# Kernel tuning notes

Hardware: AMD Instinct MI355X
Metric: run time of the kernel (lower is better)

The kernel has to match this reference:

```python
import jax, jax.numpy as jnp
import numpy as np

N = 1_000_000
D_IN = 128
D_OUT = 64
NUM_CLASSES = 64


def setup_inputs() -> dict:
    key = jax.random.key(0)
    k1, k2, k3, k4 = jax.random.split(key, 4)
    inputs = jax.random.normal(k1, (N, D_IN), dtype=jnp.float32)
    labels = jax.random.randint(k2, (N,), 0, NUM_CLASSES, dtype=jnp.int32)
    # Linear embedding parameters
    W = jax.random.normal(k3, (D_IN, D_OUT), dtype=jnp.float32) / np.sqrt(D_IN)
    b = jax.random.normal(k4, (D_OUT,), dtype=jnp.float32) * 0.01
    return {"inputs": inputs, "labels": labels, "W": W, "b": b}


def reference(inputs, labels, W, b):
    # embedding: simple linear map  [N, D_IN] -> [N, D_OUT]
    emb = jnp.einsum("nd,de->ne", inputs, W) + b
    # per-class mean pooling (prototype): segment sum / segment count
    seg_sum = jax.ops.segment_sum(emb, labels, num_segments=NUM_CLASSES)  # [C, D_OUT]
    counts = jax.ops.segment_sum(jnp.ones((inputs.shape[0],), dtype=emb.dtype),
                                 labels, num_segments=NUM_CLASSES)  # [C]
    protos = seg_sum / jnp.maximum(counts, 1.0)[:, None]
    return protos
```

## Files before the change

### kernel.cpp

```cpp
#include <hip/hip_runtime.h>

#define C_CLASSES 64
#define D_IN 128
#define D_OUT 64
#define CHUNK 32
#define CHUNK_FLTS (CHUNK * D_IN)
#define GSUM_FLTS (C_CLASSES * D_IN)
#define NBLK 1024


typedef __attribute__((ext_vector_type(8))) __bf16 bf16x8;
typedef __attribute__((ext_vector_type(8))) unsigned short us8;
typedef __attribute__((ext_vector_type(4))) float f32x4;

union frag_cast { us8 u; bf16x8 b; };

__device__ __forceinline__ unsigned short f2bf(float f) {
    unsigned u = __float_as_uint(f);
    unsigned r = u + 0x7FFFu + ((u >> 16) & 1u);
    return (unsigned short)(r >> 16);
}

__device__ __forceinline__ void stage16(const float* g, float* l) {
    __builtin_amdgcn_global_load_lds(
        (const __attribute__((address_space(1))) unsigned int*)g,
        (__attribute__((address_space(3))) unsigned int*)l, 16, 0, 0);
}

__global__ __launch_bounds__(256) void seg_mm_kernel(
    const float* __restrict__ x, const int* __restrict__ labels,
    float* __restrict__ gsum, float* __restrict__ partials, int n)
{
    __shared__ float buf[2][CHUNK_FLTS];

    const int lane = threadIdx.x & 63;
    const int wave = threadIdx.x >> 6;
    const int n16  = lane & 15;
    const int quad = lane >> 4;
    const int cb   = wave * 32;

    f32x4 acc[4][2];
#pragma unroll
    for (int t = 0; t < 4; ++t)
#pragma unroll
        for (int u = 0; u < 2; ++u)
            acc[t][u] = (f32x4){0.f, 0.f, 0.f, 0.f};

    const int stride = (int)gridDim.x * CHUNK;
    const int rb0    = (int)blockIdx.x * CHUNK;
    const int lslice = wave * 256;
    const int gslice = lslice + lane * 4;

#pragma unroll
    for (int r = 0; r < 4; ++r)
        stage16(x + (size_t)rb0 * D_IN + r * 1024 + gslice,
                &buf[0][r * 1024 + lslice]);
    int4 pl0 = *(const int4*)(labels + rb0 + quad * 8);
    int4 pl1 = *(const int4*)(labels + rb0 + quad * 8 + 4);

    int bufi = 0;
    for (int rb = rb0; rb < n; rb += stride, bufi ^= 1) {
        const int rbn = rb + stride;
        const bool hasNext = rbn < n;
        int4 pn0, pn1;
        if (hasNext) {
#pragma unroll
            for (int r = 0; r < 4; ++r)
                stage16(x + (size_t)rbn * D_IN + r * 1024 + gslice,
                        &buf[bufi ^ 1][r * 1024 + lslice]);
            pn0 = *(const int4*)(labels + rbn + quad * 8);
            pn1 = *(const int4*)(labels + rbn + quad * 8 + 4);
        }

        if (hasNext) {
            asm volatile("s_waitcnt vmcnt(6)\n\ts_barrier" ::: "memory");
        } else {
            asm volatile("s_waitcnt vmcnt(0)\n\ts_barrier" ::: "memory");
        }

        const int labv[8] = {pl0.x, pl0.y, pl0.z, pl0.w,
                             pl1.x, pl1.y, pl1.z, pl1.w};

        const float* lb = &buf[bufi][(quad * 8) * D_IN + cb + n16];
        frag_cast bfrag[2];
#pragma unroll
        for (int u = 0; u < 2; ++u)
#pragma unroll
            for (int j = 0; j < 8; ++j)
                bfrag[u].u[j] = f2bf(lb[j * D_IN + u * 16]);

        frag_cast afrag[4];
#pragma unroll
        for (int t = 0; t < 4; ++t)
#pragma unroll
            for (int j = 0; j < 8; ++j)
                afrag[t].u[j] = (labv[j] == t * 16 + n16)
                                    ? (unsigned short)0x3F80u : (unsigned short)0u;

#pragma unroll
        for (int t = 0; t < 4; ++t)
#pragma unroll
            for (int u = 0; u < 2; ++u)
                acc[t][u] = __builtin_amdgcn_mfma_f32_16x16x32_bf16(
                    afrag[t].b, bfrag[u].b, acc[t][u], 0, 0, 0);

        asm volatile("s_barrier" ::: "memory");

        if (hasNext) { pl0 = pn0; pl1 = pn1; }
    }

    if (partials) {
        float* prow = partials + (size_t)blockIdx.x * GSUM_FLTS;
#pragma unroll
        for (int t = 0; t < 4; ++t)
#pragma unroll
            for (int u = 0; u < 2; ++u)
#pragma unroll
                for (int r = 0; r < 4; ++r)
                    prow[(t * 16 + quad * 4 + r) * D_IN + cb + u * 16 + n16] =
                        acc[t][u][r];
    } else {
#pragma unroll
        for (int t = 0; t < 4; ++t)
#pragma unroll
            for (int u = 0; u < 2; ++u)
#pragma unroll
                for (int r = 0; r < 4; ++r)
                    unsafeAtomicAdd(
                        &gsum[(t * 16 + quad * 4 + r) * D_IN + cb + u * 16 + n16],
                        acc[t][u][r]);
    }
}

__global__ __launch_bounds__(256) void reduce_kernel(
    const float* __restrict__ partials, float* __restrict__ gsum)
{
    const int t   = (int)(blockIdx.x * blockDim.x + threadIdx.x);
    const int col = t & (GSUM_FLTS - 1);
    const int pg  = t >> 13;
    float a = 0.f;
#pragma unroll 8
    for (int p = 0; p < NBLK / 8; ++p)
        a += partials[(size_t)(pg * (NBLK / 8) + p) * GSUM_FLTS + col];
    unsafeAtomicAdd(&gsum[col], a);
}

__global__ __launch_bounds__(256) void count_kernel(
    const int* __restrict__ labels, float* __restrict__ gcnt, int n)
{
    const int lane = threadIdx.x & 63;
    const int gw   = (int)(blockIdx.x * blockDim.x + threadIdx.x) >> 6;
    const int nw   = (int)(gridDim.x * blockDim.x) >> 6;

    int cnt = 0;
    for (int base = gw * 64; base < n; base += nw * 64) {
        const int lab = labels[base + lane];
#pragma unroll
        for (int c = 0; c < C_CLASSES; ++c) {
            unsigned long long m = __ballot(lab == c);
            cnt += (lane == c) ? __popcll(m) : 0;
        }
    }
    unsafeAtomicAdd(&gcnt[lane], (float)cnt);
}

__global__ __launch_bounds__(256) void proto_kernel(
    const float* __restrict__ gsum, const float* __restrict__ gcnt,
    const float* __restrict__ W, const float* __restrict__ b,
    float* __restrict__ out)
{
    const int t = (int)(blockIdx.x * blockDim.x + threadIdx.x);
    const int c = t >> 6;
    const int e = t & 63;

    const float* srow = gsum + (c << 7);
    float acc = 0.0f;
#pragma unroll
    for (int k = 0; k < D_IN; ++k)
        acc = fmaf(srow[k], W[k * D_OUT + e], acc);

    const float cnt = gcnt[c];
    out[(c << 6) + e] = (acc + cnt * b[e]) / fmaxf(cnt, 1.0f);
}

extern "C" void kernel_launch(void* const* d_in, const int* in_sizes, int n_in,
                              void* d_out, int out_size, void* d_ws, size_t ws_size,
                              hipStream_t stream)
{
    const float* x      = (const float*)d_in[0];
    const int*   labels = (const int*)d_in[1];
    const float* W      = (const float*)d_in[2];
    const float* b      = (const float*)d_in[3];
    float*       out    = (float*)d_out;

    float* gsum = (float*)d_ws;
    float* gcnt = gsum + GSUM_FLTS;
    float* partials = gcnt + C_CLASSES;

    const int n = in_sizes[0] / D_IN;

    const size_t need = (size_t)(GSUM_FLTS + C_CLASSES) * sizeof(float)
                      + (size_t)NBLK * GSUM_FLTS * sizeof(float);
    const bool use_partials = ws_size >= need;

    hipMemsetAsync(d_ws, 0, (GSUM_FLTS + C_CLASSES) * sizeof(float), stream);

    seg_mm_kernel<<<NBLK, 256, 0, stream>>>(
        x, labels, gsum, use_partials ? partials : (float*)nullptr, n);

    count_kernel<<<256, 256, 0, stream>>>(labels, gcnt, n);

    if (use_partials)
        reduce_kernel<<<(8 * GSUM_FLTS) / 256, 256, 0, stream>>>(partials, gsum);

    proto_kernel<<<(C_CLASSES * D_OUT) / 256, 256, 0, stream>>>(gsum, gcnt, W, b, out);
}
```

Baseline: 715.6 us.

## Swizzle LDS staging layout, drop partials reduction, widen count grid

Staging loads now use an XOR-swizzled global offset so that rows in different 8-row groups land in LDS with a 16-float column swap, and the fragment reads undo the swap per quad. The aim is to spread LDS bank conflicts on the strided bf16 fragment reads. The partials buffer and its reduce kernel are removed, so every block atomically adds its 64x128 accumulator into gsum. The count kernel grid grows from 256 to 1024 blocks. This trades a 32 MB partials write and read for heavy atomic contention on 8K addresses.

Result: slower. 764.2 us (+6.8%).

```diff
diff --git a/kernel.cpp b/kernel.cpp
--- a/kernel.cpp
+++ b/kernel.cpp
@@ -29,7 +29,7 @@
 
 __global__ __launch_bounds__(256) void seg_mm_kernel(
     const float* __restrict__ x, const int* __restrict__ labels,
-    float* __restrict__ gsum, float* __restrict__ partials, int n)
+    float* __restrict__ gsum, int n)
 {
     __shared__ float buf[2][CHUNK_FLTS];
 
@@ -38,6 +38,7 @@
     const int n16  = lane & 15;
     const int quad = lane >> 4;
     const int cb   = wave * 32;
+    const int xu   = quad & 1;
 
     f32x4 acc[4][2];
 #pragma unroll
@@ -49,14 +50,25 @@
     const int stride = (int)gridDim.x * CHUNK;
     const int rb0    = (int)blockIdx.x * CHUNK;
     const int lslice = wave * 256;
-    const int gslice = lslice + lane * 4;
 
+    int goff[4];
 #pragma unroll
-    for (int r = 0; r < 4; ++r)
-        stage16(x + (size_t)rb0 * D_IN + r * 1024 + gslice,
-                &buf[0][r * 1024 + lslice]);
-    int4 pl0 = *(const int4*)(labels + rb0 + quad * 8);
-    int4 pl1 = *(const int4*)(labels + rb0 + quad * 8 + 4);
+    for (int r = 0; r < 4; ++r) {
+        const int o = r * 1024 + lslice + lane * 4;
+        const int k = o >> 7;
+        const int d = o & 127;
+        goff[r] = k * D_IN + (d ^ (((k >> 3) & 1) << 4));
+    }
+
+    int4 pl0 = {0,0,0,0}, pl1 = {0,0,0,0};
+    if (rb0 < n) {
+#pragma unroll
+        for (int r = 0; r < 4; ++r)
+            stage16(x + (size_t)rb0 * D_IN + goff[r],
+                    &buf[0][r * 1024 + lslice]);
+        pl0 = *(const int4*)(labels + rb0 + quad * 8);
+        pl1 = *(const int4*)(labels + rb0 + quad * 8 + 4);
+    }
 
     int bufi = 0;
     for (int rb = rb0; rb < n; rb += stride, bufi ^= 1) {
@@ -66,7 +78,7 @@
         if (hasNext) {
 #pragma unroll
             for (int r = 0; r < 4; ++r)
-                stage16(x + (size_t)rbn * D_IN + r * 1024 + gslice,
+                stage16(x + (size_t)rbn * D_IN + goff[r],
                         &buf[bufi ^ 1][r * 1024 + lslice]);
             pn0 = *(const int4*)(labels + rbn + quad * 8);
             pn1 = *(const int4*)(labels + rbn + quad * 8 + 4);
@@ -87,7 +99,7 @@
         for (int u = 0; u < 2; ++u)
 #pragma unroll
             for (int j = 0; j < 8; ++j)
-                bfrag[u].u[j] = f2bf(lb[j * D_IN + u * 16]);
+                bfrag[u].u[j] = f2bf(lb[j * D_IN + ((u ^ xu) * 16)]);
 
         frag_cast afrag[4];
 #pragma unroll
@@ -109,40 +121,15 @@
         if (hasNext) { pl0 = pn0; pl1 = pn1; }
     }
 
-    if (partials) {
-        float* prow = partials + (size_t)blockIdx.x * GSUM_FLTS;
 #pragma unroll
-        for (int t = 0; t < 4; ++t)
+    for (int t = 0; t < 4; ++t)
 #pragma unroll
-            for (int u = 0; u < 2; ++u)
+        for (int u = 0; u < 2; ++u)
 #pragma unroll
-                for (int r = 0; r < 4; ++r)
-                    prow[(t * 16 + quad * 4 + r) * D_IN + cb + u * 16 + n16] =
-                        acc[t][u][r];
-    } else {
-#pragma unroll
-        for (int t = 0; t < 4; ++t)
-#pragma unroll
-            for (int u = 0; u < 2; ++u)
-#pragma unroll
-                for (int r = 0; r < 4; ++r)
-                    unsafeAtomicAdd(
-                        &gsum[(t * 16 + quad * 4 + r) * D_IN + cb + u * 16 + n16],
-                        acc[t][u][r]);
-    }
-}
-
-__global__ __launch_bounds__(256) void reduce_kernel(
-    const float* __restrict__ partials, float* __restrict__ gsum)
-{
-    const int t   = (int)(blockIdx.x * blockDim.x + threadIdx.x);
-    const int col = t & (GSUM_FLTS - 1);
-    const int pg  = t >> 13;
-    float a = 0.f;
-#pragma unroll 8
-    for (int p = 0; p < NBLK / 8; ++p)
-        a += partials[(size_t)(pg * (NBLK / 8) + p) * GSUM_FLTS + col];
-    unsafeAtomicAdd(&gsum[col], a);
+            for (int r = 0; r < 4; ++r)
+                unsafeAtomicAdd(
+                    &gsum[(t * 16 + quad * 4 + r) * D_IN + cb + u * 16 + n16],
+                    acc[t][u][r]);
 }
 
 __global__ __launch_bounds__(256) void count_kernel(
@@ -195,23 +182,14 @@
 
     float* gsum = (float*)d_ws;
     float* gcnt = gsum + GSUM_FLTS;
-    float* partials = gcnt + C_CLASSES;
 
     const int n = in_sizes[0] / D_IN;
 
-    const size_t need = (size_t)(GSUM_FLTS + C_CLASSES) * sizeof(float)
-                      + (size_t)NBLK * GSUM_FLTS * sizeof(float);
-    const bool use_partials = ws_size >= need;
-
     hipMemsetAsync(d_ws, 0, (GSUM_FLTS + C_CLASSES) * sizeof(float), stream);
 
-    seg_mm_kernel<<<NBLK, 256, 0, stream>>>(
-        x, labels, gsum, use_partials ? partials : (float*)nullptr, n);
+    seg_mm_kernel<<<NBLK, 256, 0, stream>>>(x, labels, gsum, n);
 
-    count_kernel<<<256, 256, 0, stream>>>(labels, gcnt, n);
-
-    if (use_partials)
-        reduce_kernel<<<(8 * GSUM_FLTS) / 256, 256, 0, stream>>>(partials, gsum);
+    count_kernel<<<1024, 256, 0, stream>>>(labels, gcnt, n);
 
     proto_kernel<<<(C_CLASSES * D_OUT) / 256, 256, 0, stream>>>(gsum, gcnt, W, b, out);
 }
```
